# Performance work log

Measured on AMD Instinct MI355X. Metric: run time of the kernel, lower is better.

Reference implementation:

```python
import jax, jax.numpy as jnp
import numpy as np

B, E, D, NH, NP = 4, 32, 1024, 16, 4
LQ = E * E
DH = D // NH


def layer_norm(x, g, b, eps=1e-6):
    m = x.mean(-1, keepdims=True)
    v = ((x - m) ** 2).mean(-1, keepdims=True)
    return (x - m) / jnp.sqrt(v + eps) * g + b


def get_ref(H, W):
    # matches MSCrossAttnBlock.get_reference_points: centers normalized to [0,1], (x, y) order
    ys, xs = jnp.meshgrid((jnp.arange(H, dtype=jnp.float32) + 0.5) / H,
                          (jnp.arange(W, dtype=jnp.float32) + 0.5) / W, indexing='ij')
    return jnp.stack([xs.ravel(), ys.ravel()], -1)  # (H*W, 2)


def bilinear_sample(value_l, loc, H, W):
    # value_l: (N, nH, H*W, dh); loc: (N, Lq, nH, P, 2) normalized to [0,1]
    # replicates F.grid_sample(align_corners=False, padding_mode='zeros') with grid = 2*loc - 1
    N, Lq, nH, P, _ = loc.shape
    x = loc[..., 0] * W - 0.5
    y = loc[..., 1] * H - 0.5
    x0 = jnp.floor(x)
    y0 = jnp.floor(y)
    wx1 = x - x0
    wy1 = y - y0
    out = 0.0
    for dy, wy in ((0, 1.0 - wy1), (1, wy1)):
        for dx, wx in ((0, 1.0 - wx1), (1, wx1)):
            xi = x0 + dx
            yi = y0 + dy
            valid = (xi >= 0) & (xi < W) & (yi >= 0) & (yi < H)
            idx = (jnp.clip(yi, 0, H - 1) * W + jnp.clip(xi, 0, W - 1)).astype(jnp.int32)
            idx_t = idx.transpose(0, 2, 1, 3).reshape(N, nH, Lq * P)  # (N, nH, Lq*P)
            g = jnp.take_along_axis(value_l, idx_t[..., None], axis=2)  # (N, nH, Lq*P, dh)
            g = g.reshape(N, nH, Lq, P, -1).transpose(0, 2, 1, 3, 4)  # (N, Lq, nH, P, dh)
            w = (wx * wy) * valid.astype(value_l.dtype)
            out = out + g * w[..., None]
    return out


def msdeform(query, ref, inp, shapes, Wv, bv, Wo, bo, Wa, ba, Wp, bp):
    # MSDeformAttn forward (no padding mask)
    N, Lq, d = query.shape
    nL = len(shapes)
    value = (inp @ Wv.T + bv).reshape(N, -1, NH, DH).transpose(0, 2, 1, 3)  # (N, nH, Lin, dh)
    off = (query @ Wo.T + bo).reshape(N, Lq, NH, nL, NP, 2)
    attw = jax.nn.softmax((query @ Wa.T + ba).reshape(N, Lq, NH, nL * NP), axis=-1)
    attw = attw.reshape(N, Lq, NH, nL, NP)
    normalizer = jnp.array([[w, h] for (h, w) in shapes], dtype=query.dtype)  # (nL, 2) = [W, H]
    loc = ref[None, :, None, None, None, :] + off / normalizer[None, None, None, :, None, :]
    out = 0.0
    start = 0
    for l, (H, W) in enumerate(shapes):
        sampled = bilinear_sample(value[:, :, start:start + H * W], loc[:, :, :, l], H, W)
        out = out + (sampled * attw[:, :, :, l, :, None]).sum(3)  # (N, Lq, nH, dh)
        start += H * W
    return out.reshape(N, Lq, d) @ Wp.T + bp


def setup_inputs() -> dict:
    key = jax.random.key(0)
    ks = iter(jax.random.split(key, 64))
    def rnd(shape, scale):
        return jax.random.normal(next(ks), shape, dtype=jnp.float32) * scale
    inp = {}
    for i in range(4):
        inp[f'src{i}'] = rnd((B, LQ, D), 1.0)
    for nm in ('qn', 'fn', 'n1'):
        inp[nm + '_g'] = jnp.ones((D,), jnp.float32)
        inp[nm + '_b'] = jnp.zeros((D,), jnp.float32)
    inp['gamma1'] = rnd((D,), 0.1)
    inp['gamma2'] = rnd((D,), 0.1)
    ws = D ** -0.5
    for pre, nl in (('ca', 4), ('sa', 1)):
        inp[pre + '_vw'] = rnd((D, D), ws)
        inp[pre + '_vb'] = jnp.zeros((D,), jnp.float32)
        inp[pre + '_ow'] = rnd((NH * nl * NP * 2, D), ws)
        inp[pre + '_ob'] = rnd((NH * nl * NP * 2,), 0.1)
        inp[pre + '_aw'] = rnd((NH * nl * NP, D), ws)
        inp[pre + '_ab'] = jnp.zeros((NH * nl * NP,), jnp.float32)
        inp[pre + '_pw'] = rnd((D, D), ws)
        inp[pre + '_pb'] = jnp.zeros((D,), jnp.float32)
    return inp


def reference(src0, src1, src2, src3, qn_g, qn_b, fn_g, fn_b, n1_g, n1_b, gamma1, gamma2,
              ca_vw, ca_vb, ca_ow, ca_ob, ca_aw, ca_ab, ca_pw, ca_pb,
              sa_vw, sa_vb, sa_ow, sa_ob, sa_aw, sa_ab, sa_pw, sa_pb):
    shapes4 = [(E, E)] * 4
    feat = jnp.concatenate([src0, src1, src2, src3], axis=1)  # (B, 4*LQ, D)
    query = src3  # srcs[-1], pos embed is None
    ref = get_ref(E, E)  # (LQ, 2)
    attn = msdeform(layer_norm(query, qn_g, qn_b), ref, layer_norm(feat, fn_g, fn_b),
                    shapes4, ca_vw, ca_vb, ca_ow, ca_ob, ca_aw, ca_ab, ca_pw, ca_pb)
    attn1 = layer_norm(attn, n1_g, n1_b)
    attn2 = msdeform(attn1, ref, attn1, [(E, E)],
                     sa_vw, sa_vb, sa_ow, sa_ob, sa_aw, sa_ab, sa_pw, sa_pb)
    attn = attn + gamma2 * attn2
    return query + gamma1 * attn
```

## Files before the change

kernel.cpp:

```cpp
#include <hip/hip_runtime.h>


#define DEV __device__ __forceinline__

typedef float f32x4 __attribute__((ext_vector_type(4)));
typedef __bf16 bf16x8 __attribute__((ext_vector_type(8)));

DEV unsigned short f2bf(float f) {
  union { float f; unsigned u; } a; a.f = f;
  unsigned r = a.u + 0x7fffu + ((a.u >> 16) & 1u);
  return (unsigned short)(r >> 16);
}
DEV float bf2f(unsigned short h) {
  union { unsigned u; float f; } a; a.u = ((unsigned)h) << 16;
  return a.f;
}

struct CvtArgs {
  const float* src[8];
  unsigned short* dst;
  int off4[9];
};

__global__ __launch_bounds__(256) void f2bf_multi(CvtArgs a) {
  int i = blockIdx.x * 256 + threadIdx.x;
  int seg = 0;
  #pragma unroll
  for (int s = 1; s < 8; ++s) seg += (i >= a.off4[s]) ? 1 : 0;
  const float4 v = ((const float4*)a.src[seg])[i - a.off4[seg]];
  unsigned short* o = a.dst + (size_t)i * 4;
  o[0] = f2bf(v.x); o[1] = f2bf(v.y); o[2] = f2bf(v.z); o[3] = f2bf(v.w);
}

DEV void ln_row(const float* __restrict__ xr, const float* __restrict__ g,
                const float* __restrict__ b, unsigned short* __restrict__ op_row) {
  float4 v = ((const float4*)xr)[threadIdx.x];
  float s  = v.x + v.y + v.z + v.w;
  float s2 = v.x*v.x + v.y*v.y + v.z*v.z + v.w*v.w;
  #pragma unroll
  for (int o = 32; o; o >>= 1) { s += __shfl_down(s, o); s2 += __shfl_down(s2, o); }
  __shared__ float red[8];
  int wave = threadIdx.x >> 6, lane = threadIdx.x & 63;
  if (lane == 0) { red[wave] = s; red[4 + wave] = s2; }
  __syncthreads();
  if (threadIdx.x == 0) {
    float ts  = red[0] + red[1] + red[2] + red[3];
    float ts2 = red[4] + red[5] + red[6] + red[7];
    float mean = ts * (1.f / 1024.f);
    float var  = ts2 * (1.f / 1024.f) - mean * mean;
    red[0] = mean; red[1] = rsqrtf(var + 1e-6f);
  }
  __syncthreads();
  float mean = red[0], rstd = red[1];
  float4 gg = ((const float4*)g)[threadIdx.x];
  float4 bb = ((const float4*)b)[threadIdx.x];
  unsigned short* op = op_row + threadIdx.x * 4;
  op[0] = f2bf((v.x - mean) * rstd * gg.x + bb.x);
  op[1] = f2bf((v.y - mean) * rstd * gg.y + bb.y);
  op[2] = f2bf((v.z - mean) * rstd * gg.z + bb.z);
  op[3] = f2bf((v.w - mean) * rstd * gg.w + bb.w);
}

__global__ __launch_bounds__(256) void ln_bf16_kernel(
    const float* __restrict__ x, const float* __restrict__ g,
    const float* __restrict__ b, unsigned short* __restrict__ out) {
  int row = blockIdx.x;
  ln_row(x + (size_t)row * 1024, g, b, out + (size_t)row * 1024);
}

__global__ __launch_bounds__(256) void ln5_kernel(
    const float* __restrict__ s0, const float* __restrict__ s1,
    const float* __restrict__ s2, const float* __restrict__ s3,
    const float* __restrict__ fg, const float* __restrict__ fb,
    const float* __restrict__ qg, const float* __restrict__ qb,
    unsigned short* __restrict__ f_out, unsigned short* __restrict__ q_out) {
  int blk = blockIdx.x;
  int seg = blk >> 12, inner = blk & 4095;
  if (seg < 4) {
    const float* srcs[4] = {s0, s1, s2, s3};
    int orow = (inner >> 10) * 4096 + seg * 1024 + (inner & 1023);
    ln_row(srcs[seg] + (size_t)inner * 1024, fg, fb,
           f_out + (size_t)orow * 1024);
  } else {
    ln_row(s3 + (size_t)inner * 1024, qg, qb, q_out + (size_t)inner * 1024);
  }
}

struct GemmP {
  const unsigned short* A; const unsigned short* W;
  void* C; void* C1; void* C2;
  const float* b0; const float* b1; const float* b2;
  const float* src3; const float* g1; const float* g2; const float* attnp;
  int M, N, K, tilesM;
};

template <int BM, int BN, int EPI>
__global__ __launch_bounds__(256) void gemm_v3(GemmP P) {
  constexpr int WMT = BM / 2, WNT = BN / 2;
  constexpr int MF = WMT / 16, NF = WNT / 16;
  constexpr int PA = BM / 64, PB = BN / 64;
  __shared__ __align__(16) unsigned short sA[BM * 64];
  __shared__ __align__(16) unsigned short sB[BN * 64];
  const int tid = threadIdx.x;
  const int wave = tid >> 6, lane = tid & 63;
  const int wm = (wave & 1) * WMT, wn = (wave >> 1) * WNT;
  const int id = blockIdx.x;
  const int m0 = (id % P.tilesM) * BM;
  const int n0 = (id / P.tilesM) * BN;
  const int lq = lane >> 4, lm = lane & 15;
  const int r16 = lane >> 2;
  const int cst = lane & 3;
  const int csrc = cst ^ ((r16 >> 1) & 3);
  const int aslot = lq ^ ((lm >> 1) & 3);

  f32x4 acc[MF][NF] = {};
  bf16x8 ald[2][PA], bld[2][PB];

  #pragma unroll 1
  for (int k0 = 0; k0 < P.K; k0 += 64) {
    #pragma unroll
    for (int s = 0; s < 2; ++s) {
      #pragma unroll
      for (int p = 0; p < PA; ++p) {
        int grow = m0 + (wave + 4 * p) * 16 + r16;
        ald[s][p] = *(const bf16x8*)(P.A + (size_t)grow * P.K + k0 + s * 32 + csrc * 8);
      }
      #pragma unroll
      for (int p = 0; p < PB; ++p) {
        int grow = min(n0 + (wave + 4 * p) * 16 + r16, P.N - 1);
        bld[s][p] = *(const bf16x8*)(P.W + (size_t)grow * P.K + k0 + s * 32 + csrc * 8);
      }
    }
    __syncthreads();
    #pragma unroll
    for (int s = 0; s < 2; ++s) {
      #pragma unroll
      for (int p = 0; p < PA; ++p)
        *(bf16x8*)(sA + s * BM * 32 + (wave + 4 * p) * 512 + (r16 * 4 + cst) * 8) = ald[s][p];
      #pragma unroll
      for (int p = 0; p < PB; ++p)
        *(bf16x8*)(sB + s * BN * 32 + (wave + 4 * p) * 512 + (r16 * 4 + cst) * 8) = bld[s][p];
    }
    __syncthreads();
    #pragma unroll
    for (int s = 0; s < 2; ++s) {
      bf16x8 af[MF], bfr[NF];
      #pragma unroll
      for (int mi = 0; mi < MF; ++mi)
        af[mi] = *(const bf16x8*)(sA + s * BM * 32 + ((wm >> 4) + mi) * 512 + lm * 32 + aslot * 8);
      #pragma unroll
      for (int ni = 0; ni < NF; ++ni)
        bfr[ni] = *(const bf16x8*)(sB + s * BN * 32 + ((wn >> 4) + ni) * 512 + lm * 32 + aslot * 8);
      #pragma unroll
      for (int mi = 0; mi < MF; ++mi)
        #pragma unroll
        for (int ni = 0; ni < NF; ++ni)
          acc[mi][ni] = __builtin_amdgcn_mfma_f32_16x16x32_bf16(
              af[mi], bfr[ni], acc[mi][ni], 0, 0, 0);
    }
  }

  #pragma unroll
  for (int mi = 0; mi < MF; ++mi) {
    #pragma unroll
    for (int ni = 0; ni < NF; ++ni) {
      const int col = n0 + wn + ni * 16 + lm;
      #pragma unroll
      for (int r2 = 0; r2 < 4; ++r2) {
        const int row = m0 + wm + mi * 16 + lq * 4 + r2;
        float v = acc[mi][ni][r2];
        if constexpr (EPI == 0) {
          ((float*)P.C)[(size_t)row * 1024 + col] = v + P.b0[col];
        } else if constexpr (EPI == 1) {
          ((unsigned short*)P.C)[(size_t)row * 1024 + col] = f2bf(v + P.b0[col]);
        } else if constexpr (EPI == 2) {
          if (col < 512)
            ((float*)P.C)[(size_t)row * 512 + col] = v + P.b0[col];
          else
            ((float*)P.C1)[(size_t)row * 256 + col - 512] = v + P.b1[col - 512];
        } else if constexpr (EPI == 3) {
          if (col < 1024)
            ((unsigned short*)P.C)[(size_t)row * 1024 + col] = f2bf(v + P.b0[col]);
          else if (col < 1152)
            ((float*)P.C1)[(size_t)row * 128 + col - 1024] = v + P.b1[col - 1024];
          else if (col < 1216)
            ((float*)P.C2)[(size_t)row * 64 + col - 1152] = v + P.b2[col - 1152];
        } else {
          size_t i = (size_t)row * 1024 + col;
          float vv = v + P.b0[col];
          ((float*)P.C)[i] = P.src3[i] + P.g1[col] * (P.attnp[i] + P.g2[col] * vv);
        }
      }
    }
  }
}

template <int NLEV>
__global__ __launch_bounds__(256) void ms_sample_fused(
    const unsigned short* __restrict__ value, const float* __restrict__ off,
    const float* __restrict__ logits, unsigned short* __restrict__ out) {
  const int nq = blockIdx.x;
  const int wave = threadIdx.x >> 6, lane = threadIdx.x & 63;
  const int h = (wave << 2) + (lane >> 4);
  const int c = (lane & 15) << 2;
  const int q = nq & 1023, n = nq >> 10;
  const float* offp = off + ((size_t)nq * 16 + h) * (NLEV * 8);
  const float* lgp  = logits + ((size_t)nq * 16 + h) * (NLEV * 4);

  float lg[NLEV * 4];
  #pragma unroll
  for (int i = 0; i < NLEV; ++i) {
    float4 v = ((const float4*)lgp)[i];
    lg[4*i] = v.x; lg[4*i+1] = v.y; lg[4*i+2] = v.z; lg[4*i+3] = v.w;
  }
  float mx = lg[0];
  #pragma unroll
  for (int i = 1; i < NLEV * 4; ++i) mx = fmaxf(mx, lg[i]);
  float ssum = 0.f;
  #pragma unroll
  for (int i = 0; i < NLEV * 4; ++i) { lg[i] = __expf(lg[i] - mx); ssum += lg[i]; }
  const float inv = 1.f / ssum;

  const float fqx = (float)(q & 31), fqy = (float)(q >> 5);
  float a0 = 0.f, a1 = 0.f, a2 = 0.f, a3 = 0.f;

  #pragma unroll
  for (int l = 0; l < NLEV; ++l) {
    const unsigned short* vl =
        value + ((size_t)(n * NLEV + l) << 20) + h * 64 + c;
    #pragma unroll
    for (int p = 0; p < 4; ++p) {
      float2 o2 = ((const float2*)offp)[l * 4 + p];
      float aw = lg[l * 4 + p] * inv;
      float xx = fqx + o2.x, yy = fqy + o2.y;
      float xf = floorf(xx), yf = floorf(yy);
      float fx = xx - xf, fy = yy - yf;
      int ix = (int)xf, iy = (int)yf;
      int ix1 = ix + 1, iy1 = iy + 1;
      float vx0 = ((unsigned)ix  < 32u) ? 1.f : 0.f;
      float vx1 = ((unsigned)ix1 < 32u) ? 1.f : 0.f;
      float vy0 = ((unsigned)iy  < 32u) ? 1.f : 0.f;
      float vy1 = ((unsigned)iy1 < 32u) ? 1.f : 0.f;
      int cx0 = min(max(ix, 0), 31), cx1 = min(max(ix1, 0), 31);
      int cy0 = min(max(iy, 0), 31), cy1 = min(max(iy1, 0), 31);
      float w00 = (1.f - fx) * (1.f - fy) * vx0 * vy0 * aw;
      float w01 = fx * (1.f - fy) * vx1 * vy0 * aw;
      float w10 = (1.f - fx) * fy * vx0 * vy1 * aw;
      float w11 = fx * fy * vx1 * vy1 * aw;
      ushort4 u00 = *(const ushort4*)(vl + ((size_t)(cy0 * 32 + cx0) << 10));
      ushort4 u01 = *(const ushort4*)(vl + ((size_t)(cy0 * 32 + cx1) << 10));
      ushort4 u10 = *(const ushort4*)(vl + ((size_t)(cy1 * 32 + cx0) << 10));
      ushort4 u11 = *(const ushort4*)(vl + ((size_t)(cy1 * 32 + cx1) << 10));
      a0 += w00 * bf2f(u00.x) + w01 * bf2f(u01.x) + w10 * bf2f(u10.x) + w11 * bf2f(u11.x);
      a1 += w00 * bf2f(u00.y) + w01 * bf2f(u01.y) + w10 * bf2f(u10.y) + w11 * bf2f(u11.y);
      a2 += w00 * bf2f(u00.z) + w01 * bf2f(u01.z) + w10 * bf2f(u10.z) + w11 * bf2f(u11.z);
      a3 += w00 * bf2f(u00.w) + w01 * bf2f(u01.w) + w10 * bf2f(u10.w) + w11 * bf2f(u11.w);
    }
  }
  ushort4 r;
  r.x = f2bf(a0); r.y = f2bf(a1); r.z = f2bf(a2); r.w = f2bf(a3);
  *(ushort4*)(out + ((size_t)nq * 16 + h) * 64 + c) = r;
}

extern "C" void kernel_launch(void* const* d_in, const int* in_sizes, int n_in,
                              void* d_out, int out_size, void* d_ws,
                              size_t ws_size, hipStream_t stream) {
  (void)in_sizes; (void)n_in; (void)out_size; (void)ws_size;
  const float* src[4] = {(const float*)d_in[0], (const float*)d_in[1],
                         (const float*)d_in[2], (const float*)d_in[3]};
  const float* qn_g = (const float*)d_in[4];
  const float* qn_b = (const float*)d_in[5];
  const float* fn_g = (const float*)d_in[6];
  const float* fn_b = (const float*)d_in[7];
  const float* n1_g = (const float*)d_in[8];
  const float* n1_b = (const float*)d_in[9];
  const float* gamma1 = (const float*)d_in[10];
  const float* gamma2 = (const float*)d_in[11];
  const float* ca_vw = (const float*)d_in[12];
  const float* ca_vb = (const float*)d_in[13];
  const float* ca_ow = (const float*)d_in[14];
  const float* ca_ob = (const float*)d_in[15];
  const float* ca_aw = (const float*)d_in[16];
  const float* ca_ab = (const float*)d_in[17];
  const float* ca_pw = (const float*)d_in[18];
  const float* ca_pb = (const float*)d_in[19];
  const float* sa_vw = (const float*)d_in[20];
  const float* sa_vb = (const float*)d_in[21];
  const float* sa_ow = (const float*)d_in[22];
  const float* sa_ob = (const float*)d_in[23];
  const float* sa_aw = (const float*)d_in[24];
  const float* sa_ab = (const float*)d_in[25];
  const float* sa_pw = (const float*)d_in[26];
  const float* sa_pb = (const float*)d_in[27];

  char* wsp = (char*)d_ws;
  size_t off = 0;
  auto alloc = [&](size_t bytes) {
    char* r = wsp + off;
    off = (off + bytes + 255) & ~(size_t)255;
    return r;
  };
  const size_t MB = 1024 * 1024;
  unsigned short* w_ca_vw = (unsigned short*)alloc(1024 * 1024 * 2);
  unsigned short* w_ca_ow = (unsigned short*)alloc(512 * 1024 * 2);
  unsigned short* w_ca_aw = (unsigned short*)alloc(256 * 1024 * 2);
  unsigned short* w_ca_pw = (unsigned short*)alloc(1024 * 1024 * 2);
  unsigned short* w_sa_vw = (unsigned short*)alloc(1024 * 1024 * 2);
  unsigned short* w_sa_ow = (unsigned short*)alloc(128 * 1024 * 2);
  unsigned short* w_sa_aw = (unsigned short*)alloc(64 * 1024 * 2);
  unsigned short* w_sa_pw = (unsigned short*)alloc(1024 * 1024 * 2);
  (void)w_ca_aw; (void)w_sa_ow; (void)w_sa_aw;
  char* R1 = alloc(32 * MB);
  char* R2 = alloc(32 * MB);
  char* R3 = alloc(8 * MB);
  char* R4 = alloc(8 * MB);
  char* R5 = alloc(4 * MB);

  unsigned short* f_ln    = (unsigned short*)R1;
  float*          attn    = (float*)R1;
  unsigned short* attn1   = (unsigned short*)(R1 + 16 * MB);
  unsigned short* samp_sa = (unsigned short*)(R1 + 24 * MB);
  unsigned short* val_ca  = (unsigned short*)R2;
  unsigned short* val_sa  = (unsigned short*)R2;
  unsigned short* q_ln    = (unsigned short*)R3;
  unsigned short* samp_ca = (unsigned short*)R3;
  float*          off_ca  = (float*)R4;
  float*          off_sa  = (float*)R4;
  float*          attw_sa = (float*)(R4 + 4 * MB);
  float*          attw_ca = (float*)R5;

  CvtArgs ca;
  ca.src[0] = ca_vw; ca.src[1] = ca_ow; ca.src[2] = ca_aw; ca.src[3] = ca_pw;
  ca.src[4] = sa_vw; ca.src[5] = sa_ow; ca.src[6] = sa_aw; ca.src[7] = sa_pw;
  ca.dst = w_ca_vw;
  const int sizes4[8] = {262144, 131072, 65536, 262144, 262144, 32768, 16384, 262144};
  ca.off4[0] = 0;
  for (int i = 0; i < 8; ++i) ca.off4[i + 1] = ca.off4[i] + sizes4[i];
  f2bf_multi<<<ca.off4[8] / 256, 256, 0, stream>>>(ca);

  ln5_kernel<<<20480, 256, 0, stream>>>(src[0], src[1], src[2], src[3],
                                        fn_g, fn_b, qn_g, qn_b, f_ln, q_ln);

  auto mkP = [](const unsigned short* A, const unsigned short* W, void* C,
                const float* b0, int M, int N, int K, int tilesM) {
    GemmP p{}; p.A = A; p.W = W; p.C = C; p.b0 = b0;
    p.M = M; p.N = N; p.K = K; p.tilesM = tilesM;
    return p;
  };

  gemm_v3<128, 128, 1><<<128 * 8, 256, 0, stream>>>(
      mkP(f_ln, w_ca_vw, val_ca, ca_vb, 16384, 1024, 1024, 128));
  {
    GemmP p = mkP(q_ln, w_ca_ow, off_ca, ca_ob, 4096, 768, 1024, 64);
    p.C1 = attw_ca; p.b1 = ca_ab;
    gemm_v3<64, 128, 2><<<64 * 6, 256, 0, stream>>>(p);
  }

  ms_sample_fused<4><<<4096, 256, 0, stream>>>(val_ca, off_ca, attw_ca, samp_ca);
  gemm_v3<64, 128, 0><<<64 * 8, 256, 0, stream>>>(
      mkP(samp_ca, w_ca_pw, attn, ca_pb, 4096, 1024, 1024, 64));

  ln_bf16_kernel<<<4096, 256, 0, stream>>>(attn, n1_g, n1_b, attn1);
  {
    GemmP p = mkP(attn1, w_sa_vw, val_sa, sa_vb, 4096, 1216, 1024, 64);
    p.C1 = off_sa; p.b1 = sa_ob; p.C2 = attw_sa; p.b2 = sa_ab;
    gemm_v3<64, 128, 3><<<64 * 10, 256, 0, stream>>>(p);
  }
  ms_sample_fused<1><<<4096, 256, 0, stream>>>(val_sa, off_sa, attw_sa, samp_sa);
  {
    GemmP p = mkP(samp_sa, w_sa_pw, d_out, sa_pb, 4096, 1024, 1024, 64);
    p.src3 = src[3]; p.g1 = gamma1; p.g2 = gamma2; p.attnp = attn;
    gemm_v3<64, 128, 4><<<64 * 8, 256, 0, stream>>>(p);
  }
}
```

Before: 366.6 us.

## Use wave-per-row layernorm and merge value/offset GEMMs into one launch

LayerNorm kernels now give each 64-lane wave one row, reducing across the wave with xor shuffles instead of a block-wide shared-memory reduction with two barriers, and writing packed ushort4 stores. The cross-attention value projection and the offset/attention-weight projection are merged into a single dual-mode GEMM launch, so their blocks run concurrently and fill the device better than the small offset GEMM does alone. The offset GEMM now uses 128x128 tiles, and shared memory becomes dynamic. The risks are more register pressure in the wave-per-row LN and a different tile shape for the offset GEMM.

```diff
diff --git a/kernel.cpp b/kernel.cpp
--- a/kernel.cpp
+++ b/kernel.cpp
@@ -32,57 +32,59 @@
   o[0] = f2bf(v.x); o[1] = f2bf(v.y); o[2] = f2bf(v.z); o[3] = f2bf(v.w);
 }
 
-DEV void ln_row(const float* __restrict__ xr, const float* __restrict__ g,
-                const float* __restrict__ b, unsigned short* __restrict__ op_row) {
-  float4 v = ((const float4*)xr)[threadIdx.x];
-  float s  = v.x + v.y + v.z + v.w;
-  float s2 = v.x*v.x + v.y*v.y + v.z*v.z + v.w*v.w;
-  #pragma unroll
-  for (int o = 32; o; o >>= 1) { s += __shfl_down(s, o); s2 += __shfl_down(s2, o); }
-  __shared__ float red[8];
-  int wave = threadIdx.x >> 6, lane = threadIdx.x & 63;
-  if (lane == 0) { red[wave] = s; red[4 + wave] = s2; }
-  __syncthreads();
-  if (threadIdx.x == 0) {
-    float ts  = red[0] + red[1] + red[2] + red[3];
-    float ts2 = red[4] + red[5] + red[6] + red[7];
-    float mean = ts * (1.f / 1024.f);
-    float var  = ts2 * (1.f / 1024.f) - mean * mean;
-    red[0] = mean; red[1] = rsqrtf(var + 1e-6f);
-  }
-  __syncthreads();
-  float mean = red[0], rstd = red[1];
-  float4 gg = ((const float4*)g)[threadIdx.x];
-  float4 bb = ((const float4*)b)[threadIdx.x];
-  unsigned short* op = op_row + threadIdx.x * 4;
-  op[0] = f2bf((v.x - mean) * rstd * gg.x + bb.x);
-  op[1] = f2bf((v.y - mean) * rstd * gg.y + bb.y);
-  op[2] = f2bf((v.z - mean) * rstd * gg.z + bb.z);
-  op[3] = f2bf((v.w - mean) * rstd * gg.w + bb.w);
-}
-
-__global__ __launch_bounds__(256) void ln_bf16_kernel(
+DEV void ln_row_wave(const float* __restrict__ xr, const float* __restrict__ g,
+                     const float* __restrict__ b,
+                     unsigned short* __restrict__ op_row) {
+  const int lane = threadIdx.x & 63;
+  float4 v[4];
+  float s = 0.f, s2 = 0.f;
+  #pragma unroll
+  for (int j = 0; j < 4; ++j) {
+    v[j] = ((const float4*)xr)[lane + 64 * j];
+    s  += v[j].x + v[j].y + v[j].z + v[j].w;
+    s2 += v[j].x*v[j].x + v[j].y*v[j].y + v[j].z*v[j].z + v[j].w*v[j].w;
+  }
+  #pragma unroll
+  for (int o = 32; o; o >>= 1) { s += __shfl_xor(s, o); s2 += __shfl_xor(s2, o); }
+  const float mean = s * (1.f / 1024.f);
+  const float rstd = rsqrtf(s2 * (1.f / 1024.f) - mean * mean + 1e-6f);
+  #pragma unroll
+  for (int j = 0; j < 4; ++j) {
+    float4 gg = ((const float4*)g)[lane + 64 * j];
+    float4 bb = ((const float4*)b)[lane + 64 * j];
+    ushort4 r;
+    r.x = f2bf((v[j].x - mean) * rstd * gg.x + bb.x);
+    r.y = f2bf((v[j].y - mean) * rstd * gg.y + bb.y);
+    r.z = f2bf((v[j].z - mean) * rstd * gg.z + bb.z);
+    r.w = f2bf((v[j].w - mean) * rstd * gg.w + bb.w);
+    ((ushort4*)op_row)[lane + 64 * j] = r;
+  }
+}
+
+__global__ __launch_bounds__(256) void ln_wave_kernel(
     const float* __restrict__ x, const float* __restrict__ g,
     const float* __restrict__ b, unsigned short* __restrict__ out) {
-  int row = blockIdx.x;
-  ln_row(x + (size_t)row * 1024, g, b, out + (size_t)row * 1024);
-}
-
-__global__ __launch_bounds__(256) void ln5_kernel(
+  int row = blockIdx.x * 4 + (threadIdx.x >> 6);
+  ln_row_wave(x + (size_t)row * 1024, g, b, out + (size_t)row * 1024);
+}
+
+__global__ __launch_bounds__(256) void ln5_wave_kernel(
     const float* __restrict__ s0, const float* __restrict__ s1,
     const float* __restrict__ s2, const float* __restrict__ s3,
     const float* __restrict__ fg, const float* __restrict__ fb,
     const float* __restrict__ qg, const float* __restrict__ qb,
     unsigned short* __restrict__ f_out, unsigned short* __restrict__ q_out) {
-  int blk = blockIdx.x;
-  int seg = blk >> 12, inner = blk & 4095;
-  if (seg < 4) {
+  int row = blockIdx.x * 4 + (threadIdx.x >> 6);
+  if (row < 16384) {
+    int l = row >> 12, inner = row & 4095;
     const float* srcs[4] = {s0, s1, s2, s3};
-    int orow = (inner >> 10) * 4096 + seg * 1024 + (inner & 1023);
-    ln_row(srcs[seg] + (size_t)inner * 1024, fg, fb,
-           f_out + (size_t)orow * 1024);
+    int orow = (inner >> 10) * 4096 + l * 1024 + (inner & 1023);
+    ln_row_wave(srcs[l] + (size_t)inner * 1024, fg, fb,
+                f_out + (size_t)orow * 1024);
   } else {
-    ln_row(s3 + (size_t)inner * 1024, qg, qb, q_out + (size_t)inner * 1024);
+    int inner = row - 16384;
+    ln_row_wave(s3 + (size_t)inner * 1024, qg, qb,
+                q_out + (size_t)inner * 1024);
   }
 }
 
@@ -95,16 +97,14 @@
 };
 
 template <int BM, int BN, int EPI>
-__global__ __launch_bounds__(256) void gemm_v3(GemmP P) {
+DEV void gemm_body(const GemmP& P, int id, unsigned short* sA,
+                   unsigned short* sB) {
   constexpr int WMT = BM / 2, WNT = BN / 2;
   constexpr int MF = WMT / 16, NF = WNT / 16;
   constexpr int PA = BM / 64, PB = BN / 64;
-  __shared__ __align__(16) unsigned short sA[BM * 64];
-  __shared__ __align__(16) unsigned short sB[BN * 64];
   const int tid = threadIdx.x;
   const int wave = tid >> 6, lane = tid & 63;
   const int wm = (wave & 1) * WMT, wn = (wave >> 1) * WNT;
-  const int id = blockIdx.x;
   const int m0 = (id % P.tilesM) * BM;
   const int n0 = (id / P.tilesM) * BN;
   const int lq = lane >> 4, lm = lane & 15;
@@ -193,6 +193,21 @@
       }
     }
   }
+}
+
+template <int BM, int BN, int EPI>
+__global__ __launch_bounds__(256) void gemm_v3(GemmP P) {
+  extern __shared__ __align__(16) unsigned short smem[];
+  gemm_body<BM, BN, EPI>(P, blockIdx.x, smem, smem + BM * 64);
+}
+
+template <int BM, int BN>
+__global__ __launch_bounds__(256) void gemm_dual(GemmP Pv, GemmP Po, int split) {
+  extern __shared__ __align__(16) unsigned short smem[];
+  if ((int)blockIdx.x < split)
+    gemm_body<BM, BN, 1>(Pv, blockIdx.x, smem, smem + BM * 64);
+  else
+    gemm_body<BM, BN, 2>(Po, blockIdx.x - split, smem, smem + BM * 64);
 }
 
 template <int NLEV>
@@ -338,8 +353,8 @@
   for (int i = 0; i < 8; ++i) ca.off4[i + 1] = ca.off4[i] + sizes4[i];
   f2bf_multi<<<ca.off4[8] / 256, 256, 0, stream>>>(ca);
 
-  ln5_kernel<<<20480, 256, 0, stream>>>(src[0], src[1], src[2], src[3],
-                                        fn_g, fn_b, qn_g, qn_b, f_ln, q_ln);
+  ln5_wave_kernel<<<5120, 256, 0, stream>>>(src[0], src[1], src[2], src[3],
+                                            fn_g, fn_b, qn_g, qn_b, f_ln, q_ln);
 
   auto mkP = [](const unsigned short* A, const unsigned short* W, void* C,
                 const float* b0, int M, int N, int K, int tilesM) {
@@ -348,28 +363,27 @@
     return p;
   };
 
-  gemm_v3<128, 128, 1><<<128 * 8, 256, 0, stream>>>(
-      mkP(f_ln, w_ca_vw, val_ca, ca_vb, 16384, 1024, 1024, 128));
   {
-    GemmP p = mkP(q_ln, w_ca_ow, off_ca, ca_ob, 4096, 768, 1024, 64);
-    p.C1 = attw_ca; p.b1 = ca_ab;
-    gemm_v3<64, 128, 2><<<64 * 6, 256, 0, stream>>>(p);
+    GemmP pv = mkP(f_ln, w_ca_vw, val_ca, ca_vb, 16384, 1024, 1024, 128);
+    GemmP po = mkP(q_ln, w_ca_ow, off_ca, ca_ob, 4096, 768, 1024, 32);
+    po.C1 = attw_ca; po.b1 = ca_ab;
+    gemm_dual<128, 128><<<1024 + 192, 256, 65536 / 2, stream>>>(pv, po, 1024);
   }
 
   ms_sample_fused<4><<<4096, 256, 0, stream>>>(val_ca, off_ca, attw_ca, samp_ca);
-  gemm_v3<64, 128, 0><<<64 * 8, 256, 0, stream>>>(
+  gemm_v3<64, 128, 0><<<64 * 8, 256, (64 + 128) * 64 * 2, stream>>>(
       mkP(samp_ca, w_ca_pw, attn, ca_pb, 4096, 1024, 1024, 64));
 
-  ln_bf16_kernel<<<4096, 256, 0, stream>>>(attn, n1_g, n1_b, attn1);
+  ln_wave_kernel<<<1024, 256, 0, stream>>>(attn, n1_g, n1_b, attn1);
   {
     GemmP p = mkP(attn1, w_sa_vw, val_sa, sa_vb, 4096, 1216, 1024, 64);
     p.C1 = off_sa; p.b1 = sa_ob; p.C2 = attw_sa; p.b2 = sa_ab;
-    gemm_v3<64, 128, 3><<<64 * 10, 256, 0, stream>>>(p);
+    gemm_v3<64, 128, 3><<<64 * 10, 256, (64 + 128) * 64 * 2, stream>>>(p);
   }
   ms_sample_fused<1><<<4096, 256, 0, stream>>>(val_sa, off_sa, attw_sa, samp_sa);
   {
     GemmP p = mkP(samp_sa, w_sa_pw, d_out, sa_pb, 4096, 1024, 1024, 64);
     p.src3 = src[3]; p.g1 = gamma1; p.g2 = gamma2; p.attnp = attn;
-    gemm_v3<64, 128, 4><<<64 * 8, 256, 0, stream>>>(p);
-  }
-}
+    gemm_v3<64, 128, 4><<<64 * 8, 256, (64 + 128) * 64 * 2, stream>>>(p);
+  }
+}
```

Result: faster. 357.0 us (-2.6%).
